# Optimization experiments

Measured on AMD Instinct MI355X. Metric: run time of the kernel, lower is better.

The kernel has to match this reference:

```python
import jax, jax.numpy as jnp
import numpy as np

N, E, R = 50000, 800000, 8
EMB, PROJ, H, OUT = 512, 256, 256, 200


def rgcn_conv(x, src, dst, rel, W, root, bias):
    # PyG RGCNConv: per-relation linear transform, mean aggregation per relation
    # over incoming edges, summed across relations, plus root transform + bias.
    n = x.shape[0]
    r, _, out_dim = W.shape
    h = jnp.einsum('ni,rio->nro', x, W)            # [N,R,out] per-relation transforms
    msgs = h[src, rel]                             # [E,out] gather per-edge messages
    seg = dst * r + rel                            # combined (node, relation) segment id
    sums = jax.ops.segment_sum(msgs, seg, num_segments=n * r)
    cnt = jax.ops.segment_sum(jnp.ones((src.shape[0],), x.dtype), seg, num_segments=n * r)
    mean = sums / jnp.maximum(cnt, 1.0)[:, None]
    agg = mean.reshape(n, r, out_dim).sum(axis=1)  # sum over relations
    return agg + x @ root + bias


def setup_inputs() -> dict:
    key = jax.random.key(0)
    ks = jax.random.split(key, 16)
    inp = {
        'embeddings': jax.random.normal(ks[0], (N, EMB), jnp.float32),
        'node_indices': jnp.arange(N, dtype=jnp.int64) if jax.config.jax_enable_x64 else jnp.arange(N, dtype=jnp.int32),
        'src': jax.random.randint(ks[1], (E,), 0, N),
        'dst': jax.random.randint(ks[2], (E,), 0, N),
        'rel': jax.random.randint(ks[3], (E,), 0, R),
        'neg_src': jax.random.randint(ks[4], (E,), 0, N),
        'neg_dst': jax.random.randint(ks[5], (E,), 0, N),
        'neg_rel': jax.random.randint(ks[6], (E,), 0, R),
        # learned parameters
        'Wp': jax.random.normal(ks[7], (EMB, PROJ), jnp.float32) * 0.04,
        'bp': jnp.zeros((PROJ,), jnp.float32),
        'W0': jax.random.normal(ks[8], (R, PROJ, H), jnp.float32) * 0.06,
        'root0': jax.random.normal(ks[9], (PROJ, H), jnp.float32) * 0.06,
        'b0': jnp.zeros((H,), jnp.float32),
        'W1': jax.random.normal(ks[10], (R, H, H), jnp.float32) * 0.06,
        'root1': jax.random.normal(ks[11], (H, H), jnp.float32) * 0.06,
        'b1': jnp.zeros((H,), jnp.float32),
        'W2': jax.random.normal(ks[12], (R, H, OUT), jnp.float32) * 0.06,
        'root2': jax.random.normal(ks[13], (H, OUT), jnp.float32) * 0.06,
        'b2': jnp.zeros((OUT,), jnp.float32),
        'rel_emb': jax.random.normal(ks[14], (R, OUT), jnp.float32),
    }
    return inp


def reference(embeddings, node_indices, src, dst, rel, neg_src, neg_dst, neg_rel,
              Wp, bp, W0, root0, b0, W1, root1, b1, W2, root2, b2, rel_emb):
    # projection: Linear per modality, then reorder rows by node index (sort)
    proj = embeddings @ Wp + bp                        # [N,PROJ]
    x = jnp.zeros_like(proj).at[node_indices].set(proj)
    # stacked RGCN encoder with relu between layers (no relu on last)
    x = jax.nn.relu(rgcn_conv(x, src, dst, rel, W0, root0, b0))
    x = jax.nn.relu(rgcn_conv(x, src, dst, rel, W1, root1, b1))
    out = rgcn_conv(x, src, dst, rel, W2, root2, b2)   # [N,OUT]
    # DistMult decoder over positive + negative triples
    s = jnp.concatenate([src, neg_src])
    o = jnp.concatenate([dst, neg_dst])
    r = jnp.concatenate([rel, neg_rel])
    scores = jnp.sum(out[s] * rel_emb[r] * out[o], axis=-1)  # [2E]
    return out, scores
```

## Files before the change

### kernel.cpp

```cpp
#include <hip/hip_runtime.h>
#include <stdint.h>

#define NN 50000
#define NE 800000
#define NR 8
#define EMBD 512
#define PROJD 256
#define HIDD 256
#define OUTD 200
#define NSEG (NN * NR)
#define CSR_CAP 1536

typedef _Float16 half8 __attribute__((ext_vector_type(8)));
typedef _Float16 half4 __attribute__((ext_vector_type(4)));
typedef float f32x4 __attribute__((ext_vector_type(4)));

__device__ __forceinline__ void gload16(const void* g, void* l) {
    __builtin_amdgcn_global_load_lds(
        reinterpret_cast<const __attribute__((address_space(1))) uint32_t*>(
            reinterpret_cast<uintptr_t>(g)),
        reinterpret_cast<__attribute__((address_space(3))) uint32_t*>(
            reinterpret_cast<uintptr_t>(l)),
        16, 0, 0);
}


__global__ void count_edges(const int* __restrict__ dst, const int* __restrict__ rel,
                            int* __restrict__ cnt, int E) {
    int e = blockIdx.x * 256 + threadIdx.x;
    if (e >= E) return;
    atomicAdd(&cnt[dst[e] * NR + rel[e]], 1);
}

__global__ __launch_bounds__(512) void scan1(const int* __restrict__ cnt, int* __restrict__ offs,
                                             int* __restrict__ bsums, int n) {
    __shared__ int sm[512];
    int tid = threadIdx.x;
    int g = blockIdx.x * 512 + tid;
    int v = (g < n) ? cnt[g] : 0;
    sm[tid] = v;
    __syncthreads();
    for (int o = 1; o < 512; o <<= 1) {
        int t = (tid >= o) ? sm[tid - o] : 0;
        __syncthreads();
        sm[tid] += t;
        __syncthreads();
    }
    if (g < n) offs[g] = sm[tid] - v;
    if (tid == 511) bsums[blockIdx.x] = sm[511];
}

__global__ __launch_bounds__(1024) void scan2(const int* __restrict__ bsums, int* __restrict__ bpref, int nb) {
    __shared__ int sm[1024];
    int tid = threadIdx.x;
    int v = (tid < nb) ? bsums[tid] : 0;
    sm[tid] = v;
    __syncthreads();
    for (int o = 1; o < 1024; o <<= 1) {
        int t = (tid >= o) ? sm[tid - o] : 0;
        __syncthreads();
        sm[tid] += t;
        __syncthreads();
    }
    if (tid < nb) bpref[tid] = sm[tid] - v;
}

__global__ __launch_bounds__(512) void scan3(int* __restrict__ offs, int* __restrict__ cursor,
                                             const int* __restrict__ bpref, int n, int total) {
    int g = blockIdx.x * 512 + threadIdx.x;
    if (g < n) {
        int v = offs[g] + bpref[blockIdx.x];
        offs[g] = v;
        cursor[g] = v;
    }
    if (g == 0) offs[n] = total;
}

__global__ void pad_offs(int* __restrict__ offs, int total) {
    offs[NSEG + 1 + blockIdx.x * 256 + threadIdx.x] = total;
}

__global__ void scatter_edges(const int* __restrict__ dst, const int* __restrict__ rel,
                              const int* __restrict__ src, int* __restrict__ cursor,
                              int* __restrict__ csr, int E) {
    int e = blockIdx.x * 256 + threadIdx.x;
    if (e >= E) return;
    int seg = dst[e] * NR + rel[e];
    int pos = atomicAdd(&cursor[seg], 1);
    csr[pos] = src[e];
}


__global__ void f32_to_f16_vec(const float* __restrict__ in, _Float16* __restrict__ out, long n4) {
    long i = (long)blockIdx.x * 256 + threadIdx.x;
    long stride = (long)gridDim.x * 256;
    for (; i < n4; i += stride) {
        float4 v = ((const float4*)in)[i];
        half4 h;
        h[0] = (_Float16)v.x; h[1] = (_Float16)v.y; h[2] = (_Float16)v.z; h[3] = (_Float16)v.w;
        ((half4*)out)[i] = h;
    }
}

__global__ void build_bt(const float* __restrict__ S0, int K0, const float* __restrict__ S1,
                         _Float16* __restrict__ Bt, int N, int K) {
    int k = blockIdx.x * 256 + threadIdx.x;
    int n = blockIdx.y;
    if (k >= K) return;
    float v = (k < K0) ? S0[(size_t)k * N + n] : S1[(size_t)(k - K0) * N + n];
    Bt[(size_t)n * K + k] = (_Float16)v;
}


template <bool RELU, bool LAST>
__global__ __launch_bounds__(512, 4) void rgcn_layer(
    const _Float16* __restrict__ x, const _Float16* __restrict__ Bt,
    const int* __restrict__ csr, const int* __restrict__ offs,
    const float* __restrict__ bias,
    _Float16* __restrict__ C16, int ldc, float* __restrict__ C32, int N) {
    __shared__ _Float16 As[64 * 256];
    __shared__ _Float16 Bs[2][256 * 32];
    __shared__ int offs_lds[520];
    __shared__ int csr_lds[CSR_CAP];
    const int tid = threadIdx.x;
    const int lane = tid & 63, wave = tid >> 6;
    const int lane32 = tid & 31, hw = tid >> 5;
    const int half_base = lane & 32;
    const int l15 = lane & 15, q = lane >> 4;
    const int wm = wave >> 2, wn = wave & 3;
    const int m0 = blockIdx.x * 64;
    const int segbase = m0 * NR;

    for (int i = tid; i < 513; i += 512) offs_lds[i] = offs[segbase + i];
    __syncthreads();
    const int e0 = offs_lds[0];
    const int e1 = offs_lds[512];
    const int ecnt = min(e1 - e0, CSR_CAP);
    for (int i = tid; i < ecnt; i += 512) csr_lds[i] = csr[e0 + i];
    __syncthreads();

    auto stage = [&](int buf, int g) {
        int kbase = g * 32;
#pragma unroll
        for (int h = 0; h < 2; ++h) {
            int s = tid + h * 512;
            int n = s >> 2, c4 = s & 3;
            int nn = n < N ? n : N - 1;
            gload16(Bt + (size_t)nn * 2304 + kbase + ((c4 ^ (n & 3)) << 3),
                    &Bs[buf][(size_t)(wave * 64 + h * 512) * 8]);
        }
    };

    f32x4 acc[2][4] = {};
    stage(0, 0);
    int cur = 0;
    for (int seg = 0; seg < 9; ++seg) {
#pragma unroll
        for (int u = 0; u < 4; ++u) {
            int lr = u * 16 + hw;
            int nd = m0 + lr;
            if (nd >= NN) nd = NN - 1;
            half8 hv;
            if (seg == 0) {
                hv = *(const half8*)(x + (size_t)nd * 256 + lane32 * 8);
            } else {
                int sb = lr * NR + seg - 1;
                int o0 = offs_lds[sb], o1 = offs_lds[sb + 1];
                int n = o1 - o0;
                if (n < 0) n = 0;
                if (n == 0) {
#pragma unroll
                    for (int z = 0; z < 8; ++z) hv[z] = (_Float16)0.f;
                } else {
                    bool staged = (o1 - e0) <= CSR_CAP;
                    int fi = o0 + (lane32 < n ? lane32 : n - 1);
                    int idxv = staged ? csr_lds[fi - e0] : csr[fi];
                    float a0=0.f,a1=0.f,a2=0.f,a3=0.f,a4=0.f,a5=0.f,a6=0.f,a7=0.f;
                    int nb = n < 32 ? n : 32;
                    for (int e = 0; e < nb; e += 2) {
                        int s0 = __shfl(idxv, half_base + e);
                        half8 v0 = *(const half8*)(x + (size_t)s0 * 256 + lane32 * 8);
                        if (e + 1 < nb) {
                            int s1 = __shfl(idxv, half_base + e + 1);
                            half8 v1 = *(const half8*)(x + (size_t)s1 * 256 + lane32 * 8);
                            a0 += (float)v0[0] + (float)v1[0];
                            a1 += (float)v0[1] + (float)v1[1];
                            a2 += (float)v0[2] + (float)v1[2];
                            a3 += (float)v0[3] + (float)v1[3];
                            a4 += (float)v0[4] + (float)v1[4];
                            a5 += (float)v0[5] + (float)v1[5];
                            a6 += (float)v0[6] + (float)v1[6];
                            a7 += (float)v0[7] + (float)v1[7];
                        } else {
                            a0 += (float)v0[0]; a1 += (float)v0[1];
                            a2 += (float)v0[2]; a3 += (float)v0[3];
                            a4 += (float)v0[4]; a5 += (float)v0[5];
                            a6 += (float)v0[6]; a7 += (float)v0[7];
                        }
                    }
                    for (int e = 32; e < n; ++e) {
                        int s2 = staged ? csr_lds[o0 - e0 + e] : csr[o0 + e];
                        half8 v = *(const half8*)(x + (size_t)s2 * 256 + lane32 * 8);
                        a0 += (float)v[0]; a1 += (float)v[1];
                        a2 += (float)v[2]; a3 += (float)v[3];
                        a4 += (float)v[4]; a5 += (float)v[5];
                        a6 += (float)v[6]; a7 += (float)v[7];
                    }
                    float inv = 1.0f / (float)n;
                    hv[0] = (_Float16)(a0 * inv); hv[1] = (_Float16)(a1 * inv);
                    hv[2] = (_Float16)(a2 * inv); hv[3] = (_Float16)(a3 * inv);
                    hv[4] = (_Float16)(a4 * inv); hv[5] = (_Float16)(a5 * inv);
                    hv[6] = (_Float16)(a6 * inv); hv[7] = (_Float16)(a7 * inv);
                }
            }
            *(half8*)((char*)As + lr * 512 + ((lane32 ^ (lr & 31)) << 4)) = hv;
        }
        asm volatile("s_waitcnt lgkmcnt(0)" ::: "memory");
        __builtin_amdgcn_s_barrier();
        asm volatile("" ::: "memory");
        for (int ch = 0; ch < 8; ++ch) {
            int g = seg * 8 + ch;
            if (g < 71) {
                stage(cur ^ 1, g + 1);
                asm volatile("s_waitcnt vmcnt(2)" ::: "memory");
            } else {
                asm volatile("s_waitcnt vmcnt(0)" ::: "memory");
            }
            __builtin_amdgcn_s_barrier();
            asm volatile("" ::: "memory");
            half8 a[2], b[4];
#pragma unroll
            for (int i = 0; i < 2; ++i) {
                int row = wm * 32 + i * 16 + l15;
                int ck = ch * 4 + q;
                a[i] = *(const half8*)((const char*)As + row * 512 + ((ck ^ (row & 31)) << 4));
            }
#pragma unroll
            for (int j = 0; j < 4; ++j) {
                int n = wn * 64 + j * 16 + l15;
                b[j] = *(const half8*)((const char*)&Bs[cur][0] + n * 64 + ((q ^ (n & 3)) << 4));
            }
#pragma unroll
            for (int i = 0; i < 2; ++i)
#pragma unroll
                for (int j = 0; j < 4; ++j)
                    acc[i][j] = __builtin_amdgcn_mfma_f32_16x16x32_f16(a[i], b[j], acc[i][j], 0, 0, 0);
            asm volatile("s_waitcnt lgkmcnt(0)" ::: "memory");
            __builtin_amdgcn_s_barrier();
            asm volatile("" ::: "memory");
            cur ^= 1;
        }
    }
#pragma unroll
    for (int i = 0; i < 2; ++i) {
        int rbase = m0 + wm * 32 + i * 16 + q * 4;
#pragma unroll
        for (int j = 0; j < 4; ++j) {
            int cc = wn * 64 + j * 16 + l15;
            if (cc >= N) continue;
            float bv = bias[cc];
#pragma unroll
            for (int t = 0; t < 4; ++t) {
                int rr = rbase + t;
                if (rr >= NN) continue;
                float v = acc[i][j][t] + bv;
                if (RELU) v = fmaxf(v, 0.f);
                C16[(size_t)rr * ldc + cc] = (_Float16)v;
                if (LAST) C32[(size_t)rr * ldc + cc] = v;
            }
        }
    }
}


template <bool BIAS, bool ACC_IN, bool FINAL, bool RELU, bool LAST, bool SCATTER>
__global__ __launch_bounds__(256) void gemm16(
    const _Float16* __restrict__ A, int lda,
    const _Float16* __restrict__ Bt, int ldb,
    const float* __restrict__ bias, const int* __restrict__ sidx,
    _Float16* __restrict__ Cacc,
    _Float16* __restrict__ C16, int ldc, float* __restrict__ C32,
    int M, int N, int K) {
    __shared__ _Float16 As[2][4096];
    __shared__ _Float16 Bs[2][4096];
    const int tid = threadIdx.x;
    const int lane = tid & 63, wave = tid >> 6;
    const int wm = wave >> 1, wn = wave & 1;
    const int q = lane >> 4, l15 = lane & 15;
    const int m0 = blockIdx.y * 128, n0 = blockIdx.x * 128;
    const int wbase = wave * 512;
    f32x4 acc[4][4] = {};

    auto stage = [&](int buf, int k0) {
#pragma unroll
        for (int h = 0; h < 2; ++h) {
            int s = tid + h * 256;
            int r = s >> 2, c = s & 3;
            int cs = c ^ ((r >> 2) & 3);
            int ga = m0 + r; if (ga >= M) ga = M - 1;
            gload16(A + (size_t)ga * lda + k0 + cs * 8, &As[buf][wbase + h * 2048]);
            int gb = n0 + r; if (gb >= N) gb = N - 1;
            gload16(Bt + (size_t)gb * ldb + k0 + cs * 8, &Bs[buf][wbase + h * 2048]);
        }
    };

    const int nk = K >> 5;
    stage(0, 0);
    int cur = 0;
    for (int kt = 0; kt < nk; ++kt) {
        if (kt + 1 < nk) {
            stage(cur ^ 1, (kt + 1) << 5);
            asm volatile("s_waitcnt vmcnt(4)" ::: "memory");
        } else {
            asm volatile("s_waitcnt vmcnt(0)" ::: "memory");
        }
        __builtin_amdgcn_s_barrier();
        asm volatile("" ::: "memory");
        half8 a[4], b[4];
#pragma unroll
        for (int i = 0; i < 4; ++i) {
            int row = wm * 64 + i * 16 + l15;
            a[i] = *(const half8*)&As[cur][row * 32 + ((q ^ ((row >> 2) & 3)) << 3)];
            int col = wn * 64 + i * 16 + l15;
            b[i] = *(const half8*)&Bs[cur][col * 32 + ((q ^ ((col >> 2) & 3)) << 3)];
        }
#pragma unroll
        for (int i = 0; i < 4; ++i)
#pragma unroll
            for (int j = 0; j < 4; ++j)
                acc[i][j] = __builtin_amdgcn_mfma_f32_16x16x32_f16(a[i], b[j], acc[i][j], 0, 0, 0);
        asm volatile("s_waitcnt lgkmcnt(0)" ::: "memory");
        __builtin_amdgcn_s_barrier();
        asm volatile("" ::: "memory");
        cur ^= 1;
    }
#pragma unroll
    for (int i = 0; i < 4; ++i) {
        int rbase = m0 + wm * 64 + i * 16 + q * 4;
#pragma unroll
        for (int j = 0; j < 4; ++j) {
            int cc = n0 + wn * 64 + j * 16 + l15;
            if (cc >= N) continue;
#pragma unroll
            for (int t = 0; t < 4; ++t) {
                int rr = rbase + t;
                if (rr >= M) continue;
                float v = acc[i][j][t];
                if (BIAS) v += bias[cc];
                if (ACC_IN) v += (float)Cacc[(size_t)rr * 256 + cc];
                if (!FINAL) {
                    Cacc[(size_t)rr * 256 + cc] = (_Float16)v;
                } else {
                    if (RELU) v = fmaxf(v, 0.f);
                    int ro = SCATTER ? sidx[rr] : rr;
                    C16[(size_t)ro * ldc + cc] = (_Float16)v;
                    if (LAST) C32[(size_t)ro * ldc + cc] = v;
                }
            }
        }
    }
}


__global__ __launch_bounds__(256) void decoder16(
    const _Float16* __restrict__ out16, const _Float16* __restrict__ rel16,
    const int* __restrict__ src, const int* __restrict__ dst, const int* __restrict__ rel,
    const int* __restrict__ nsrc, const int* __restrict__ ndst, const int* __restrict__ nrel,
    float* __restrict__ scores) {
    int gid = blockIdx.x * 256 + threadIdx.x;
    int t = gid >> 4, lq = gid & 15;
    if (t >= 2 * NE) return;
    int s, o, r;
    if (t < NE) { s = src[t]; o = dst[t]; r = rel[t]; }
    else { int u = t - NE; s = nsrc[u]; o = ndst[u]; r = nrel[u]; }
    const half8* ps = (const half8*)(out16 + (size_t)s * OUTD);
    const half8* po = (const half8*)(out16 + (size_t)o * OUTD);
    const half8* pr = (const half8*)(rel16 + (size_t)r * OUTD);
    float acc = 0.f;
#pragma unroll
    for (int it = 0; it < 2; ++it) {
        int c = it * 16 + lq;
        if (c < 25) {
            half8 a = ps[c], b = pr[c], d = po[c];
#pragma unroll
            for (int u = 0; u < 8; ++u) acc += (float)a[u] * (float)b[u] * (float)d[u];
        }
    }
#pragma unroll
    for (int off = 8; off; off >>= 1) acc += __shfl_xor(acc, off);
    if (lq == 0) scores[t] = acc;
}


extern "C" void kernel_launch(void* const* d_in, const int* in_sizes, int n_in,
                              void* d_out, int out_size, void* d_ws, size_t ws_size,
                              hipStream_t stream) {
    const float* emb   = (const float*)d_in[0];
    const int*   nidx  = (const int*)d_in[1];
    const int*   src   = (const int*)d_in[2];
    const int*   dst   = (const int*)d_in[3];
    const int*   rel   = (const int*)d_in[4];
    const int*   nsrc  = (const int*)d_in[5];
    const int*   ndst  = (const int*)d_in[6];
    const int*   nrel  = (const int*)d_in[7];
    const float* Wp    = (const float*)d_in[8];
    const float* bp    = (const float*)d_in[9];
    const float* W0    = (const float*)d_in[10];
    const float* root0 = (const float*)d_in[11];
    const float* b0    = (const float*)d_in[12];
    const float* W1    = (const float*)d_in[13];
    const float* root1 = (const float*)d_in[14];
    const float* b1    = (const float*)d_in[15];
    const float* W2    = (const float*)d_in[16];
    const float* root2 = (const float*)d_in[17];
    const float* b2    = (const float*)d_in[18];
    const float* rele  = (const float*)d_in[19];
    (void)in_sizes; (void)n_in; (void)out_size; (void)ws_size;

    float* out    = (float*)d_out;
    float* scores = out + (size_t)NN * OUTD;

    auto align = [](size_t x) { return (x + 255) & ~(size_t)255; };
    char* p = (char*)d_ws;
    auto alloc = [&](size_t bytes) -> char* {
        char* q = p; p += align(bytes); return q;
    };
    _Float16* emb16  = (_Float16*)alloc((size_t)NN * EMBD * 2);
    _Float16* xbufA  = (_Float16*)alloc((size_t)NN * 256 * 2);
    _Float16* xbufB  = (_Float16*)alloc((size_t)NN * 256 * 2);
    _Float16* out16  = xbufB;
    _Float16* Bt0 = (_Float16*)alloc((size_t)256 * 2304 * 2);
    _Float16* Bt1 = (_Float16*)alloc((size_t)256 * 2304 * 2);
    _Float16* Bt2 = (_Float16*)alloc((size_t)256 * 2304 * 2);
    _Float16* BtP = (_Float16*)alloc((size_t)256 * EMBD * 2);
    _Float16* rel16 = (_Float16*)alloc((size_t)NR * OUTD * 2);
    int*   cnt    = (int*)alloc((size_t)NSEG * 4);
    int*   cursor = (int*)alloc((size_t)NSEG * 4);
    int*   offs   = (int*)alloc((size_t)(NSEG + 1032) * 4);
    int*   csr    = (int*)alloc((size_t)NE * 4);
    int*   bsums  = (int*)alloc(4096);
    int*   bpref  = (int*)alloc(4096);

    hipMemsetAsync(cnt, 0, (size_t)NSEG * 4, stream);
    count_edges<<<(NE + 255) / 256, 256, 0, stream>>>(dst, rel, cnt, NE);
    const int NB = (NSEG + 511) / 512;
    scan1<<<NB, 512, 0, stream>>>(cnt, offs, bsums, NSEG);
    scan2<<<1, 1024, 0, stream>>>(bsums, bpref, NB);
    scan3<<<NB, 512, 0, stream>>>(offs, cursor, bpref, NSEG, NE);
    pad_offs<<<4, 256, 0, stream>>>(offs, NE);
    scatter_edges<<<(NE + 255) / 256, 256, 0, stream>>>(dst, rel, src, cursor, csr, NE);

    f32_to_f16_vec<<<2048, 256, 0, stream>>>(emb, emb16, (long)NN * EMBD / 4);
    f32_to_f16_vec<<<2, 256, 0, stream>>>(rele, rel16, (long)NR * OUTD / 4);
    build_bt<<<dim3(2, 256), 256, 0, stream>>>(Wp, EMBD, nullptr, BtP, PROJD, EMBD);
    build_bt<<<dim3(9, 256), 256, 0, stream>>>(root0, 256, W0, Bt0, HIDD, 2304);
    build_bt<<<dim3(9, 256), 256, 0, stream>>>(root1, 256, W1, Bt1, HIDD, 2304);
    build_bt<<<dim3(9, 200), 256, 0, stream>>>(root2, 256, W2, Bt2, OUTD, 2304);

    hipMemsetAsync(xbufA, 0, (size_t)NN * 256 * 2, stream);
    {
        dim3 g(2, (NN + 127) / 128);
        gemm16<true, false, true, false, false, true><<<g, 256, 0, stream>>>(
            emb16, EMBD, BtP, EMBD, bp, nidx, nullptr, xbufA, 256, nullptr, NN, 256, EMBD);
    }

    const int GL = (NN + 63) / 64;
    rgcn_layer<true, false><<<GL, 512, 0, stream>>>(xbufA, Bt0, csr, offs, b0,
                                                    xbufB, 256, nullptr, HIDD);
    rgcn_layer<true, false><<<GL, 512, 0, stream>>>(xbufB, Bt1, csr, offs, b1,
                                                    xbufA, 256, nullptr, HIDD);
    rgcn_layer<false, true><<<GL, 512, 0, stream>>>(xbufA, Bt2, csr, offs, b2,
                                                    out16, OUTD, out, OUTD);

    decoder16<<<(2 * NE * 16 + 255) / 256, 256, 0, stream>>>(out16, rel16, src, dst, rel,
                                                             nsrc, ndst, nrel, scores);
}
```

Baseline: 910.5 us.

## Load RGCN weight fragments directly from global memory, drop LDS B staging

The fused RGCN layer kernel no longer stages weight tiles through double-buffered shared memory. Each of the 8 waves now owns a 32-column slice of the output and reads its B fragments straight from global memory (L2-resident weights), covering all 64 rows itself. With B staging gone, LDS use falls, the CSR cache shrinks, and occupancy is raised to 6 blocks per CU. To let the last layer read 256 columns safely, the padding rows of its transposed weight are zeroed first. In exchange, every wave now reloads weights from global/L2 with no prefetch, and per-chunk barriers are replaced by per-segment syncs.

```diff
diff --git a/kernel.cpp b/kernel.cpp
--- a/kernel.cpp
+++ b/kernel.cpp
@@ -9,7 +9,7 @@
 #define HIDD 256
 #define OUTD 200
 #define NSEG (NN * NR)
-#define CSR_CAP 1536
+#define CSR_CAP 1408
 
 typedef _Float16 half8 __attribute__((ext_vector_type(8)));
 typedef _Float16 half4 __attribute__((ext_vector_type(4)));
@@ -111,15 +111,21 @@
     Bt[(size_t)n * K + k] = (_Float16)v;
 }
 
+__global__ void zero_f16(_Float16* __restrict__ p, long n8) {
+    long i = (long)blockIdx.x * 256 + threadIdx.x;
+    if (i >= n8) return;
+    half8 z = {};
+    ((half8*)p)[i] = z;
+}
+
 
 template <bool RELU, bool LAST>
-__global__ __launch_bounds__(512, 4) void rgcn_layer(
+__global__ __launch_bounds__(512, 6) void rgcn_layer(
     const _Float16* __restrict__ x, const _Float16* __restrict__ Bt,
     const int* __restrict__ csr, const int* __restrict__ offs,
     const float* __restrict__ bias,
     _Float16* __restrict__ C16, int ldc, float* __restrict__ C32, int N) {
     __shared__ _Float16 As[64 * 256];
-    __shared__ _Float16 Bs[2][256 * 32];
     __shared__ int offs_lds[520];
     __shared__ int csr_lds[CSR_CAP];
     const int tid = threadIdx.x;
@@ -127,7 +133,7 @@
     const int lane32 = tid & 31, hw = tid >> 5;
     const int half_base = lane & 32;
     const int l15 = lane & 15, q = lane >> 4;
-    const int wm = wave >> 2, wn = wave & 3;
+    const int wn = wave;
     const int m0 = blockIdx.x * 64;
     const int segbase = m0 * NR;
 
@@ -139,21 +145,10 @@
     for (int i = tid; i < ecnt; i += 512) csr_lds[i] = csr[e0 + i];
     __syncthreads();
 
-    auto stage = [&](int buf, int g) {
-        int kbase = g * 32;
-#pragma unroll
-        for (int h = 0; h < 2; ++h) {
-            int s = tid + h * 512;
-            int n = s >> 2, c4 = s & 3;
-            int nn = n < N ? n : N - 1;
-            gload16(Bt + (size_t)nn * 2304 + kbase + ((c4 ^ (n & 3)) << 3),
-                    &Bs[buf][(size_t)(wave * 64 + h * 512) * 8]);
-        }
-    };
-
-    f32x4 acc[2][4] = {};
-    stage(0, 0);
-    int cur = 0;
+    f32x4 acc[4][2] = {};
+    const _Float16* bcol0 = Bt + (size_t)(wn * 32 + l15) * 2304 + q * 8;
+    const _Float16* bcol1 = bcol0 + (size_t)16 * 2304;
+
     for (int seg = 0; seg < 9; ++seg) {
 #pragma unroll
         for (int u = 0; u < 4; ++u) {
@@ -215,50 +210,38 @@
             }
             *(half8*)((char*)As + lr * 512 + ((lane32 ^ (lr & 31)) << 4)) = hv;
         }
-        asm volatile("s_waitcnt lgkmcnt(0)" ::: "memory");
-        __builtin_amdgcn_s_barrier();
-        asm volatile("" ::: "memory");
+        __syncthreads();
+        const _Float16* bs0 = bcol0 + seg * 256;
+        const _Float16* bs1 = bcol1 + seg * 256;
+#pragma unroll
         for (int ch = 0; ch < 8; ++ch) {
-            int g = seg * 8 + ch;
-            if (g < 71) {
-                stage(cur ^ 1, g + 1);
-                asm volatile("s_waitcnt vmcnt(2)" ::: "memory");
-            } else {
-                asm volatile("s_waitcnt vmcnt(0)" ::: "memory");
-            }
-            __builtin_amdgcn_s_barrier();
-            asm volatile("" ::: "memory");
-            half8 a[2], b[4];
-#pragma unroll
-            for (int i = 0; i < 2; ++i) {
-                int row = wm * 32 + i * 16 + l15;
-                int ck = ch * 4 + q;
+            half8 b0 = *(const half8*)(bs0 + ch * 32);
+            half8 b1 = *(const half8*)(bs1 + ch * 32);
+            half8 a[4];
+            int ck = ch * 4 + q;
+#pragma unroll
+            for (int i = 0; i < 4; ++i) {
+                int row = i * 16 + l15;
                 a[i] = *(const half8*)((const char*)As + row * 512 + ((ck ^ (row & 31)) << 4));
             }
-#pragma unroll
-            for (int j = 0; j < 4; ++j) {
-                int n = wn * 64 + j * 16 + l15;
-                b[j] = *(const half8*)((const char*)&Bs[cur][0] + n * 64 + ((q ^ (n & 3)) << 4));
+            __builtin_amdgcn_s_setprio(1);
+#pragma unroll
+            for (int i = 0; i < 4; ++i) {
+                acc[i][0] = __builtin_amdgcn_mfma_f32_16x16x32_f16(a[i], b0, acc[i][0], 0, 0, 0);
+                acc[i][1] = __builtin_amdgcn_mfma_f32_16x16x32_f16(a[i], b1, acc[i][1], 0, 0, 0);
             }
-#pragma unroll
-            for (int i = 0; i < 2; ++i)
-#pragma unroll
-                for (int j = 0; j < 4; ++j)
-                    acc[i][j] = __builtin_amdgcn_mfma_f32_16x16x32_f16(a[i], b[j], acc[i][j], 0, 0, 0);
-            asm volatile("s_waitcnt lgkmcnt(0)" ::: "memory");
-            __builtin_amdgcn_s_barrier();
-            asm volatile("" ::: "memory");
-            cur ^= 1;
-        }
-    }
-#pragma unroll
-    for (int i = 0; i < 2; ++i) {
-        int rbase = m0 + wm * 32 + i * 16 + q * 4;
-#pragma unroll
-        for (int j = 0; j < 4; ++j) {
-            int cc = wn * 64 + j * 16 + l15;
-            if (cc >= N) continue;
-            float bv = bias[cc];
+            __builtin_amdgcn_s_setprio(0);
+        }
+        __syncthreads();
+    }
+#pragma unroll
+    for (int j = 0; j < 2; ++j) {
+        int cc = wn * 32 + j * 16 + l15;
+        if (cc >= N) continue;
+        float bv = bias[cc];
+#pragma unroll
+        for (int i = 0; i < 4; ++i) {
+            int rbase = m0 + i * 16 + q * 4;
 #pragma unroll
             for (int t = 0; t < 4; ++t) {
                 int rr = rbase + t;
@@ -455,6 +438,7 @@
     build_bt<<<dim3(2, 256), 256, 0, stream>>>(Wp, EMBD, nullptr, BtP, PROJD, EMBD);
     build_bt<<<dim3(9, 256), 256, 0, stream>>>(root0, 256, W0, Bt0, HIDD, 2304);
     build_bt<<<dim3(9, 256), 256, 0, stream>>>(root1, 256, W1, Bt1, HIDD, 2304);
+    zero_f16<<<(256 * 2304 / 8 + 255) / 256, 256, 0, stream>>>(Bt2, 256 * 2304 / 8);
     build_bt<<<dim3(9, 200), 256, 0, stream>>>(root2, 256, W2, Bt2, OUTD, 2304);
 
     hipMemsetAsync(xbufA, 0, (size_t)NN * 256 * 2, stream);
```

After: 1.325 ms. 1.45x slower.
